# Optimization experiments

Hardware: AMD Instinct MI355X
Metric: run time of the kernel (lower is better)

## Reference

```python
import jax, jax.numpy as jnp
import numpy as np

N = 100000
IN_C = 128
HID = 16
HEADS = 8
OUT_C = 64
E = 1600000
NEG_SLOPE = 0.2
EPS = 1e-16


def setup_inputs() -> dict:
    key = jax.random.key(0)
    ks = jax.random.split(key, 12)
    s = lambda k, shape, fan: jax.random.normal(k, shape, jnp.float32) * (1.0 / np.sqrt(fan))
    return {
        "x": jax.random.normal(ks[0], (N, IN_C), jnp.float32),
        "edge_index": jax.random.randint(ks[1], (2, E), 0, N, jnp.int64),
        # conv1 params (heads=8, concat=True)
        "W1": s(ks[2], (IN_C, HEADS * HID), IN_C),
        "a_src1": s(ks[3], (HEADS, HID), HID),
        "a_dst1": s(ks[4], (HEADS, HID), HID),
        "b1": jnp.zeros((HEADS * HID,), jnp.float32),
        # conv2 params (heads=1, concat=False)
        "W2": s(ks[5], (HEADS * HID, OUT_C), HEADS * HID),
        "a_src2": s(ks[6], (1, OUT_C), OUT_C),
        "a_dst2": s(ks[7], (1, OUT_C), OUT_C),
        "b2": jnp.zeros((OUT_C,), jnp.float32),
    }


def gat_conv(x, src, dst, W, a_src, a_dst, bias, concat):
    """PyG-style GATConv: edge softmax over incoming edges + scatter-add."""
    H, C = a_src.shape
    n = x.shape[0]
    h = (x @ W).reshape(n, H, C)                      # [N,H,C]
    asrc = jnp.einsum("nhc,hc->nh", h, a_src)          # [N,H]
    adst = jnp.einsum("nhc,hc->nh", h, a_dst)          # [N,H]
    e = jax.nn.leaky_relu(asrc[src] + adst[dst], NEG_SLOPE)  # [E,H]
    # numerically-stable segment softmax over edges sharing a destination
    m = jax.ops.segment_max(e, dst, num_segments=n)    # [N,H]
    m = jnp.where(jnp.isfinite(m), m, 0.0)
    ex = jnp.exp(e - m[dst])                           # [E,H]
    denom = jax.ops.segment_sum(ex, dst, num_segments=n)  # [N,H]
    alpha = ex / (denom[dst] + EPS)                    # [E,H]
    out = jax.ops.segment_sum(alpha[:, :, None] * h[src], dst, num_segments=n)  # [N,H,C]
    out = out.reshape(n, H * C) if concat else out.mean(axis=1)
    return out + bias


def reference(x, edge_index, W1, a_src1, a_dst1, b1, W2, a_src2, a_dst2, b2):
    n = x.shape[0]
    # PyG GATConv adds self-loops by default
    loop = jnp.arange(n, dtype=edge_index.dtype)
    src = jnp.concatenate([edge_index[0], loop])
    dst = jnp.concatenate([edge_index[1], loop])
    # dropout(p=0.6) is identity at inference
    h = jax.nn.elu(gat_conv(x, src, dst, W1, a_src1, a_dst1, b1, concat=True))
    return gat_conv(h, src, dst, W2, a_src2, a_dst2, b2, concat=False)
```

## Files before the change

kernel.cpp:

```cpp
#include <hip/hip_runtime.h>
#include <hip/hip_bf16.h>
#include <math.h>


typedef __attribute__((ext_vector_type(8))) short short8;
typedef __attribute__((ext_vector_type(4))) float f32x4;

__device__ __forceinline__ float bflo(uint u) { return __uint_as_float(u << 16); }
__device__ __forceinline__ float bfhi(uint u) { return __uint_as_float(u & 0xffff0000u); }
__device__ __forceinline__ float bf1(ushort v) { return __uint_as_float(((uint)v) << 16); }
__device__ __forceinline__ ushort f2bf(float f) {
    uint u = __float_as_uint(f);
    u += 0x7fff + ((u >> 16) & 1);
    return (ushort)(u >> 16);
}
#define LOG2E 1.44269504088896f
#define CSR_CAP 4096

__global__ __launch_bounds__(256) void k_gemm1_bhist(
    const float* __restrict__ X, const float* __restrict__ W,
    ushort* __restrict__ Y, int n,
    const int* __restrict__ dst, int e, int* __restrict__ bcount, int nbh) {
    __shared__ union {
        struct { ushort As[128][136]; ushort Ws[128][136]; } g;
        int h[1024];
    } sm;
    const int t = threadIdx.x;
    if ((int)blockIdx.x < nbh) {
        for (int i = t; i < 1024; i += 256) sm.h[i] = 0;
        __syncthreads();
        int c0 = blockIdx.x * 8192, c1 = min(c0 + 8192, e);
        for (int i = c0 + t; i < c1; i += 256) atomicAdd(&sm.h[dst[i] >> 7], 1);
        __syncthreads();
        for (int i = t; i < 1024; i += 256)
            if (sm.h[i]) atomicAdd(&bcount[i], sm.h[i]);
        return;
    }
    const int row0 = (blockIdx.x - nbh) * 128;
#pragma unroll
    for (int q = 0; q < 16; q++) {
        int idx = t + q * 256;
        int r = idx >> 5, c4 = (idx & 31) * 4;
        float4 xv = make_float4(0.f, 0.f, 0.f, 0.f);
        if (row0 + r < n) xv = *reinterpret_cast<const float4*>(&X[(size_t)(row0 + r) * 128 + c4]);
        ushort4 w4 = make_ushort4(f2bf(xv.x), f2bf(xv.y), f2bf(xv.z), f2bf(xv.w));
        *reinterpret_cast<ushort4*>(&sm.g.As[r][c4]) = w4;
    }
    for (int i = t; i < 128 * 128; i += 256) {
        int k = i >> 7, nc = i & 127;
        sm.g.Ws[nc][k] = f2bf(W[i]);
    }
    __syncthreads();
    const int w = t >> 6, l = t & 63;
    const int lr = l & 15;
    const int lk = (l >> 4) * 8;
    f32x4 acc[2][8];
#pragma unroll
    for (int m = 0; m < 2; m++)
#pragma unroll
        for (int nb = 0; nb < 8; nb++) acc[m][nb] = (f32x4){0.f, 0.f, 0.f, 0.f};
#pragma unroll
    for (int kc = 0; kc < 128; kc += 32) {
        short8 a0 = *reinterpret_cast<const short8*>(&sm.g.As[w * 32 + lr][kc + lk]);
        short8 a1 = *reinterpret_cast<const short8*>(&sm.g.As[w * 32 + 16 + lr][kc + lk]);
#pragma unroll
        for (int nb = 0; nb < 8; nb++) {
            short8 bf = *reinterpret_cast<const short8*>(&sm.g.Ws[nb * 16 + lr][kc + lk]);
            acc[0][nb] = __builtin_amdgcn_mfma_f32_16x16x32_bf16(a0, bf, acc[0][nb], 0, 0, 0);
            acc[1][nb] = __builtin_amdgcn_mfma_f32_16x16x32_bf16(a1, bf, acc[1][nb], 0, 0, 0);
        }
    }
#pragma unroll
    for (int m = 0; m < 2; m++)
#pragma unroll
        for (int j = 0; j < 4; j++) {
            int r = row0 + w * 32 + m * 16 + (l >> 4) * 4 + j;
            if (r < n) {
#pragma unroll
                for (int nb = 0; nb < 8; nb++)
                    Y[(size_t)r * 128 + nb * 16 + lr] = f2bf(acc[m][nb][j]);
            }
        }
}

__global__ __launch_bounds__(256) void k_bscan_attn1(
    const int* __restrict__ bcount, int nb, int n,
    int* __restrict__ ebase, int* __restrict__ ecur, int* __restrict__ cbase,
    const uint* __restrict__ hu, const float* __restrict__ a_src,
    const float* __restrict__ a_dst, float* __restrict__ asrc,
    float* __restrict__ adst) {
    __shared__ int ae[1024], be[1024], ac[1024], bc[1024];
    int t = threadIdx.x;
    if (blockIdx.x == 0) {
        for (int i = t; i < 1024; i += 256) {
            int v = 0, nn = 0;
            if (i < nb) {
                v = bcount[i];
                nn = min(128, n - (i << 7));
            }
            ae[i] = v;
            ac[i] = v + nn;
        }
        __syncthreads();
        int* pa = ae; int* qa = be; int* pc = ac; int* qc = bc;
        for (int off = 1; off < 1024; off <<= 1) {
            for (int i = t; i < 1024; i += 256) {
                int va = pa[i], vc = pc[i];
                if (i >= off) { va += pa[i - off]; vc += pc[i - off]; }
                qa[i] = va; qc[i] = vc;
            }
            __syncthreads();
            int* tm = pa; pa = qa; qa = tm;
            tm = pc; pc = qc; qc = tm;
        }
        for (int i = t; i < 1024; i += 256) {
            if (i < nb) {
                int ea = (i == 0) ? 0 : pa[i - 1];
                int ca = (i == 0) ? 0 : pc[i - 1];
                ebase[i] = ea; ecur[i] = ea; cbase[i] = ca;
            }
        }
        return;
    }
    int tt = (blockIdx.x - 1) * 256 + t;
    if (tt >= n * 8) return;
    int node = tt >> 3, hd = tt & 7;
    const uint* hp = hu + (size_t)node * 64 + hd * 8;
    float s1 = 0.f, s2 = 0.f;
#pragma unroll
    for (int q = 0; q < 8; q++) {
        uint u = hp[q];
        float v0 = bflo(u), v1 = bfhi(u);
        s1 = fmaf(v0, a_src[hd * 16 + 2 * q], s1);
        s1 = fmaf(v1, a_src[hd * 16 + 2 * q + 1], s1);
        s2 = fmaf(v0, a_dst[hd * 16 + 2 * q], s2);
        s2 = fmaf(v1, a_dst[hd * 16 + 2 * q + 1], s2);
    }
    asrc[tt] = s1 * LOG2E;
    adst[tt] = s2 * LOG2E;
}

__global__ __launch_bounds__(512) void k_part(const int* __restrict__ src,
                                              const int* __restrict__ dst, int e,
                                              int* __restrict__ ecur, int* __restrict__ ebuf) {
    __shared__ int h[1024];
    __shared__ int base[1024];
    int t = threadIdx.x;
    int c0 = blockIdx.x * 8192, c1 = min(c0 + 8192, e);
    for (int i = t; i < 1024; i += 512) h[i] = 0;
    __syncthreads();
    for (int i = c0 + t; i < c1; i += 512) atomicAdd(&h[dst[i] >> 7], 1);
    __syncthreads();
    for (int i = t; i < 1024; i += 512) {
        int c = h[i];
        base[i] = c ? atomicAdd(&ecur[i], c) : 0;
        h[i] = 0;
    }
    __syncthreads();
    for (int i = c0 + t; i < c1; i += 512) {
        int d = dst[i], b = d >> 7;
        int r = atomicAdd(&h[b], 1);
        ebuf[base[b] + r] = (src[i] << 7) | (d & 127);
    }
}

__global__ __launch_bounds__(256) void k_build(const int* __restrict__ ebuf,
                                               const int* __restrict__ bcount,
                                               const int* __restrict__ ebase,
                                               const int* __restrict__ cbase,
                                               int* __restrict__ rowptr,
                                               int* __restrict__ csr, int n, int nb) {
    __shared__ int cnt[128];
    __shared__ int sc[128], sc2[128];
    __shared__ int csr_l[CSR_CAP];
    int b = blockIdx.x, t = threadIdx.x;
    int n0 = b << 7;
    int nn = min(128, n - n0);
    int ec = bcount[b], eb = ebase[b], cb = cbase[b];
    if (t < 128) cnt[t] = 0;
    __syncthreads();
    for (int i = t; i < ec; i += 256) atomicAdd(&cnt[ebuf[eb + i] & 127], 1);
    __syncthreads();
    if (t < 128) sc[t] = (t < nn) ? cnt[t] + 1 : 0;
    __syncthreads();
    int* p = sc; int* q = sc2;
    for (int off = 1; off < 128; off <<= 1) {
        if (t < 128) {
            int v = p[t];
            if (t >= off) v += p[t - off];
            q[t] = v;
        }
        __syncthreads();
        int* tm = p; p = q; q = tm;
    }
    int total = p[127];
    if (total <= CSR_CAP) {
        if (t < nn) {
            int off = (t == 0) ? 0 : p[t - 1];
            rowptr[n0 + t] = cb + off;
            csr_l[off] = n0 + t;
            cnt[t] = off + 1;
        }
        __syncthreads();
        for (int i = t; i < ec; i += 256) {
            int v = ebuf[eb + i];
            int s = atomicAdd(&cnt[v & 127], 1);
            csr_l[s] = v >> 7;
        }
        __syncthreads();
        for (int i = t; i < total; i += 256) csr[cb + i] = csr_l[i];
    } else {
        if (t < nn) {
            int off = (t == 0) ? 0 : p[t - 1];
            rowptr[n0 + t] = cb + off;
            csr[cb + off] = n0 + t;
            cnt[t] = off + 1;
        }
        __syncthreads();
        for (int i = t; i < ec; i += 256) {
            int v = ebuf[eb + i];
            int s = atomicAdd(&cnt[v & 127], 1);
            csr[cb + s] = v >> 7;
        }
    }
    if (b == nb - 1 && t == 0) rowptr[n] = cb + total;
}

__global__ __launch_bounds__(256) void k_gemm2(const ushort* __restrict__ X,
                                               const float* __restrict__ W,
                                               ushort* __restrict__ Y, int n) {
    __shared__ ushort As[128][136];
    __shared__ ushort Ws[64][136];
    const int t = threadIdx.x;
    const int row0 = blockIdx.x * 128;
#pragma unroll
    for (int q = 0; q < 8; q++) {
        int idx = t + q * 256;
        int r = idx >> 4, c8 = (idx & 15) * 8;
        uint4 v = make_uint4(0u, 0u, 0u, 0u);
        if (row0 + r < n) v = *reinterpret_cast<const uint4*>(&X[(size_t)(row0 + r) * 128 + c8]);
        *reinterpret_cast<uint4*>(&As[r][c8]) = v;
    }
    for (int i = t; i < 128 * 64; i += 256) {
        int k = i >> 6, nc = i & 63;
        Ws[nc][k] = f2bf(W[i]);
    }
    __syncthreads();
    const int w = t >> 6, l = t & 63;
    const int lr = l & 15;
    const int lk = (l >> 4) * 8;
    f32x4 acc[2][4];
#pragma unroll
    for (int m = 0; m < 2; m++)
#pragma unroll
        for (int nb = 0; nb < 4; nb++) acc[m][nb] = (f32x4){0.f, 0.f, 0.f, 0.f};
#pragma unroll
    for (int kc = 0; kc < 128; kc += 32) {
        short8 a0 = *reinterpret_cast<const short8*>(&As[w * 32 + lr][kc + lk]);
        short8 a1 = *reinterpret_cast<const short8*>(&As[w * 32 + 16 + lr][kc + lk]);
#pragma unroll
        for (int nb = 0; nb < 4; nb++) {
            short8 bf = *reinterpret_cast<const short8*>(&Ws[nb * 16 + lr][kc + lk]);
            acc[0][nb] = __builtin_amdgcn_mfma_f32_16x16x32_bf16(a0, bf, acc[0][nb], 0, 0, 0);
            acc[1][nb] = __builtin_amdgcn_mfma_f32_16x16x32_bf16(a1, bf, acc[1][nb], 0, 0, 0);
        }
    }
#pragma unroll
    for (int m = 0; m < 2; m++)
#pragma unroll
        for (int j = 0; j < 4; j++) {
            int r = row0 + w * 32 + m * 16 + (l >> 4) * 4 + j;
            if (r < n) {
#pragma unroll
                for (int nb = 0; nb < 4; nb++)
                    Y[(size_t)r * 64 + nb * 16 + lr] = f2bf(acc[m][nb][j]);
            }
        }
}

__global__ void k_attn2(const uint* __restrict__ hu, const float* __restrict__ a_src,
                        const float* __restrict__ a_dst, float* __restrict__ asrc,
                        float* __restrict__ adst, int n) {
    int t = blockIdx.x * 256 + threadIdx.x;
    if (t >= n * 8) return;
    int node = t >> 3, j = t & 7;
    const uint* hp = hu + (size_t)node * 32 + j * 4;
    float s1 = 0.f, s2 = 0.f;
#pragma unroll
    for (int q = 0; q < 4; q++) {
        uint u = hp[q];
        float v0 = bflo(u), v1 = bfhi(u);
        s1 = fmaf(v0, a_src[j * 8 + 2 * q], s1);
        s1 = fmaf(v1, a_src[j * 8 + 2 * q + 1], s1);
        s2 = fmaf(v0, a_dst[j * 8 + 2 * q], s2);
        s2 = fmaf(v1, a_dst[j * 8 + 2 * q + 1], s2);
    }
#pragma unroll
    for (int o = 1; o < 8; o <<= 1) {
        s1 += __shfl_xor(s1, o);
        s2 += __shfl_xor(s2, o);
    }
    if (j == 0) { asrc[node] = s1 * LOG2E; adst[node] = s2 * LOG2E; }
}

__global__ __launch_bounds__(256) void k_agg1(
    const uint* __restrict__ hu, const float* __restrict__ asrc,
    const float* __restrict__ adst, const int* __restrict__ rowptr,
    const int* __restrict__ csr, const float* __restrict__ b1,
    uint* __restrict__ x2, int n) {
    __shared__ float P[4][512];
    int wv = threadIdx.x >> 6;
    int wid = (blockIdx.x * 256 + threadIdx.x) >> 6;
    if (wid >= n) return;
    uint lane = threadIdx.x & 63;
    uint hd = lane >> 3;
    uint sl = lane & 7;
    uint c0 = lane * 2;
    float adn = adst[(uint)wid * 8u + hd];
    int beg = rowptr[wid], end = rowptr[wid + 1];
    float s = 0.f, acc0 = 0.f, acc1 = 0.f;
    for (int base = beg; base < end; base += 64) {
        int cnt = min(64, end - base);
        int vidx = ((int)lane < cnt) ? csr[base + lane] : 0;
        int mb = (cnt + 7) >> 3;
        for (int m = 0; m < mb; m++) {
            int slot = 8 * m + (int)sl;
            int cs = csr[base + min(slot, cnt - 1)];
            float e = asrc[(uint)cs * 8u + hd] + adn;
            e = fmaxf(e, 0.2f * e);
            P[wv][slot * 8 + hd] = exp2f(e);
        }
        asm volatile("s_waitcnt lgkmcnt(0)" ::: "memory");
        int j = 0;
        for (; j + 8 <= cnt; j += 8) {
            uint s0 = __builtin_amdgcn_readlane(vidx, j);
            uint s1 = __builtin_amdgcn_readlane(vidx, j + 1);
            uint s2 = __builtin_amdgcn_readlane(vidx, j + 2);
            uint s3 = __builtin_amdgcn_readlane(vidx, j + 3);
            uint s4 = __builtin_amdgcn_readlane(vidx, j + 4);
            uint s5 = __builtin_amdgcn_readlane(vidx, j + 5);
            uint s6 = __builtin_amdgcn_readlane(vidx, j + 6);
            uint s7 = __builtin_amdgcn_readlane(vidx, j + 7);
            uint u0 = hu[s0 * 64u + lane];
            uint u1 = hu[s1 * 64u + lane];
            uint u2 = hu[s2 * 64u + lane];
            uint u3 = hu[s3 * 64u + lane];
            uint u4 = hu[s4 * 64u + lane];
            uint u5 = hu[s5 * 64u + lane];
            uint u6 = hu[s6 * 64u + lane];
            uint u7 = hu[s7 * 64u + lane];
            float q0 = P[wv][(j + 0) * 8 + hd];
            float q1 = P[wv][(j + 1) * 8 + hd];
            float q2 = P[wv][(j + 2) * 8 + hd];
            float q3 = P[wv][(j + 3) * 8 + hd];
            float q4 = P[wv][(j + 4) * 8 + hd];
            float q5 = P[wv][(j + 5) * 8 + hd];
            float q6 = P[wv][(j + 6) * 8 + hd];
            float q7 = P[wv][(j + 7) * 8 + hd];
            s += ((q0 + q1) + (q2 + q3)) + ((q4 + q5) + (q6 + q7));
            acc0 = fmaf(q0, bflo(u0), fmaf(q1, bflo(u1), acc0));
            acc0 = fmaf(q2, bflo(u2), fmaf(q3, bflo(u3), acc0));
            acc0 = fmaf(q4, bflo(u4), fmaf(q5, bflo(u5), acc0));
            acc0 = fmaf(q6, bflo(u6), fmaf(q7, bflo(u7), acc0));
            acc1 = fmaf(q0, bfhi(u0), fmaf(q1, bfhi(u1), acc1));
            acc1 = fmaf(q2, bfhi(u2), fmaf(q3, bfhi(u3), acc1));
            acc1 = fmaf(q4, bfhi(u4), fmaf(q5, bfhi(u5), acc1));
            acc1 = fmaf(q6, bfhi(u6), fmaf(q7, bfhi(u7), acc1));
        }
        for (; j < cnt; ++j) {
            uint s0 = __builtin_amdgcn_readlane(vidx, j);
            float q0 = P[wv][j * 8 + hd];
            uint u0 = hu[s0 * 64u + lane];
            s += q0;
            acc0 = fmaf(q0, bflo(u0), acc0);
            acc1 = fmaf(q0, bfhi(u0), acc1);
        }
    }
    float inv = 1.f / (s + 1e-16f);
    float o0 = acc0 * inv + b1[c0];
    float o1 = acc1 * inv + b1[c0 + 1];
    o0 = o0 > 0.f ? o0 : (__expf(o0) - 1.f);
    o1 = o1 > 0.f ? o1 : (__expf(o1) - 1.f);
    union { ushort b[2]; uint u; } pk;
    pk.b[0] = f2bf(o0);
    pk.b[1] = f2bf(o1);
    x2[(uint)wid * 64u + lane] = pk.u;
}
__global__ __launch_bounds__(256) void k_agg2(
    const ushort* __restrict__ hb, const float* __restrict__ asrc,
    const float* __restrict__ adst, const int* __restrict__ rowptr,
    const int* __restrict__ csr, const float* __restrict__ b2,
    float* __restrict__ out, int n) {
    __shared__ float P2[4][64];
    int wv = threadIdx.x >> 6;
    int wid = (blockIdx.x * 256 + threadIdx.x) >> 6;
    if (wid >= n) return;
    uint lane = threadIdx.x & 63;
    float adn = adst[wid];
    int beg = rowptr[wid], end = rowptr[wid + 1];
    float s = 0.f, acc = 0.f;
    for (int base = beg; base < end; base += 64) {
        int cnt = min(64, end - base);
        int vidx = csr[base + min((int)lane, cnt - 1)];
        float e = asrc[vidx] + adn;
        e = fmaxf(e, 0.2f * e);
        P2[wv][lane] = ((int)lane < cnt) ? exp2f(e) : 0.f;
        asm volatile("s_waitcnt lgkmcnt(0)" ::: "memory");
        int j = 0;
        for (; j + 8 <= cnt; j += 8) {
            uint s0 = __builtin_amdgcn_readlane(vidx, j);
            uint s1 = __builtin_amdgcn_readlane(vidx, j + 1);
            uint s2 = __builtin_amdgcn_readlane(vidx, j + 2);
            uint s3 = __builtin_amdgcn_readlane(vidx, j + 3);
            uint s4 = __builtin_amdgcn_readlane(vidx, j + 4);
            uint s5 = __builtin_amdgcn_readlane(vidx, j + 5);
            uint s6 = __builtin_amdgcn_readlane(vidx, j + 6);
            uint s7 = __builtin_amdgcn_readlane(vidx, j + 7);
            float h0 = bf1(hb[s0 * 64u + lane]);
            float h1 = bf1(hb[s1 * 64u + lane]);
            float h2 = bf1(hb[s2 * 64u + lane]);
            float h3 = bf1(hb[s3 * 64u + lane]);
            float h4 = bf1(hb[s4 * 64u + lane]);
            float h5 = bf1(hb[s5 * 64u + lane]);
            float h6 = bf1(hb[s6 * 64u + lane]);
            float h7 = bf1(hb[s7 * 64u + lane]);
            float q0 = P2[wv][j + 0];
            float q1 = P2[wv][j + 1];
            float q2 = P2[wv][j + 2];
            float q3 = P2[wv][j + 3];
            float q4 = P2[wv][j + 4];
            float q5 = P2[wv][j + 5];
            float q6 = P2[wv][j + 6];
            float q7 = P2[wv][j + 7];
            s += ((q0 + q1) + (q2 + q3)) + ((q4 + q5) + (q6 + q7));
            acc = fmaf(q0, h0, fmaf(q1, h1, acc));
            acc = fmaf(q2, h2, fmaf(q3, h3, acc));
            acc = fmaf(q4, h4, fmaf(q5, h5, acc));
            acc = fmaf(q6, h6, fmaf(q7, h7, acc));
        }
        for (; j < cnt; ++j) {
            uint s0 = __builtin_amdgcn_readlane(vidx, j);
            float q0 = P2[wv][j];
            float h0 = bf1(hb[s0 * 64u + lane]);
            s += q0;
            acc = fmaf(q0, h0, acc);
        }
    }
    out[(size_t)wid * 64 + lane] = acc / (s + 1e-16f) + b2[lane];
}

extern "C" void kernel_launch(void* const* d_in, const int* in_sizes, int n_in,
                              void* d_out, int out_size, void* d_ws, size_t ws_size,
                              hipStream_t stream) {
    const float* x   = (const float*)d_in[0];
    const int*   ei  = (const int*)d_in[1];
    const float* W1  = (const float*)d_in[2];
    const float* as1 = (const float*)d_in[3];
    const float* ad1 = (const float*)d_in[4];
    const float* b1  = (const float*)d_in[5];
    const float* W2  = (const float*)d_in[6];
    const float* as2 = (const float*)d_in[7];
    const float* ad2 = (const float*)d_in[8];
    const float* b2  = (const float*)d_in[9];
    float* out = (float*)d_out;

    int N = in_sizes[0] / 128;
    int E = in_sizes[1] / 2;
    int TOT = E + N;
    const int* src = ei;
    const int* dst = ei + E;

    char* p = (char*)d_ws;
    auto alloc = [&](size_t bytes) {
        char* r = p;
        p += (bytes + 255) & ~size_t(255);
        return r;
    };
    ushort* h1b  = (ushort*)alloc((size_t)N * 128 * 2);
    ushort* h2b  = (ushort*)alloc((size_t)N * 64 * 2);
    ushort* x2b  = (ushort*)alloc((size_t)N * 128 * 2);
    float* asrc1 = (float*)alloc((size_t)N * 8 * 4);
    float* adst1 = (float*)alloc((size_t)N * 8 * 4);
    float* asrc2 = (float*)alloc((size_t)N * 4);
    float* adst2 = (float*)alloc((size_t)N * 4);
    int* rowptr  = (int*)alloc((size_t)(N + 1) * 4);
    int* csr     = (int*)alloc((size_t)TOT * 4);
    int* ebuf    = (int*)alloc((size_t)E * 4);
    int* bcount  = (int*)alloc(1024 * 4);
    int* ebase   = (int*)alloc(1024 * 4);
    int* ecur    = (int*)alloc(1024 * 4);
    int* cbase   = (int*)alloc(1024 * 4);

    int NB = (N + 127) >> 7;
    int nbp = (E + 8191) / 8192;
    int gb = (N + 127) / 128;

    hipMemsetAsync(bcount, 0, 1024 * 4, stream);
    k_gemm1_bhist<<<nbp + gb, 256, 0, stream>>>(x, W1, h1b, N, dst, E, bcount, nbp);
    k_bscan_attn1<<<1 + (N * 8 + 255) / 256, 256, 0, stream>>>(
        bcount, NB, N, ebase, ecur, cbase, (const uint*)h1b, as1, ad1, asrc1, adst1);
    k_part<<<nbp, 512, 0, stream>>>(src, dst, E, ecur, ebuf);
    k_build<<<NB, 256, 0, stream>>>(ebuf, bcount, ebase, cbase, rowptr, csr, N, NB);
    k_agg1<<<(N + 3) / 4, 256, 0, stream>>>((const uint*)h1b, asrc1, adst1, rowptr, csr, b1,
                                            (uint*)x2b, N);
    k_gemm2<<<gb, 256, 0, stream>>>(x2b, W2, h2b, N);
    k_attn2<<<(N * 8 + 255) / 256, 256, 0, stream>>>((const uint*)h2b, as2, ad2, asrc2, adst2, N);
    k_agg2<<<(N + 3) / 4, 256, 0, stream>>>((const ushort*)h2b, asrc2, adst2, rowptr, csr, b2,
                                            out, N);
}
```

Measured before the change: 235.8 us.

## Precompute layer-1 edge attention weights in CSR build and store as fp16

Moves the per-edge leaky-relu and exp2 computation for layer-1 attention out of the aggregation kernel and into the CSR build kernel. Each edge writes 8 fp16 unnormalised weights in CSR order, and asrc/adst are stored as fp16 to halve their gather traffic. k_agg1 then streams those precomputed weights instead of gathering asrc per edge and staging the results in LDS. The cost is an extra E*16-byte write and read, a second shared array in k_build, and reduced precision from fp16 logits and weights, which could overflow since no max subtraction is applied.

Result: faster. 229.2 us (-2.8%).

```diff
diff --git a/kernel.cpp b/kernel.cpp
--- a/kernel.cpp
+++ b/kernel.cpp
@@ -87,8 +87,8 @@
     const int* __restrict__ bcount, int nb, int n,
     int* __restrict__ ebase, int* __restrict__ ecur, int* __restrict__ cbase,
     const uint* __restrict__ hu, const float* __restrict__ a_src,
-    const float* __restrict__ a_dst, float* __restrict__ asrc,
-    float* __restrict__ adst) {
+    const float* __restrict__ a_dst, _Float16* __restrict__ asrc,
+    _Float16* __restrict__ adst) {
     __shared__ int ae[1024], be[1024], ac[1024], bc[1024];
     int t = threadIdx.x;
     if (blockIdx.x == 0) {
@@ -136,8 +136,8 @@
         s2 = fmaf(v0, a_dst[hd * 16 + 2 * q], s2);
         s2 = fmaf(v1, a_dst[hd * 16 + 2 * q + 1], s2);
     }
-    asrc[tt] = s1 * LOG2E;
-    adst[tt] = s2 * LOG2E;
+    asrc[tt] = (_Float16)(s1 * LOG2E);
+    adst[tt] = (_Float16)(s2 * LOG2E);
 }
 
 __global__ __launch_bounds__(512) void k_part(const int* __restrict__ src,
@@ -168,11 +168,15 @@
                                                const int* __restrict__ bcount,
                                                const int* __restrict__ ebase,
                                                const int* __restrict__ cbase,
+                                               const _Float16* __restrict__ asrc,
+                                               const _Float16* __restrict__ adst,
                                                int* __restrict__ rowptr,
-                                               int* __restrict__ csr, int n, int nb) {
+                                               int* __restrict__ csr,
+                                               _Float16* __restrict__ p1, int n, int nb) {
     __shared__ int cnt[128];
     __shared__ int sc[128], sc2[128];
     __shared__ int csr_l[CSR_CAP];
+    __shared__ int dst_l[CSR_CAP];
     int b = blockIdx.x, t = threadIdx.x;
     int n0 = b << 7;
     int nn = min(128, n - n0);
@@ -199,6 +203,7 @@
             int off = (t == 0) ? 0 : p[t - 1];
             rowptr[n0 + t] = cb + off;
             csr_l[off] = n0 + t;
+            dst_l[off] = n0 + t;
             cnt[t] = off + 1;
         }
         __syncthreads();
@@ -206,21 +211,59 @@
             int v = ebuf[eb + i];
             int s = atomicAdd(&cnt[v & 127], 1);
             csr_l[s] = v >> 7;
-        }
-        __syncthreads();
-        for (int i = t; i < total; i += 256) csr[cb + i] = csr_l[i];
+            dst_l[s] = n0 + (v & 127);
+        }
+        __syncthreads();
+        for (int i = t; i < total; i += 256) {
+            int s = csr_l[i], d = dst_l[i];
+            csr[cb + i] = s;
+            const _Float16* pa = asrc + (size_t)s * 8;
+            const _Float16* pb = adst + (size_t)d * 8;
+            _Float16 buf[8];
+#pragma unroll
+            for (int h = 0; h < 8; h++) {
+                float e = (float)pa[h] + (float)pb[h];
+                e = fmaxf(e, 0.2f * e);
+                buf[h] = (_Float16)exp2f(e);
+            }
+            *reinterpret_cast<uint4*>(&p1[(size_t)(cb + i) * 8]) =
+                *reinterpret_cast<const uint4*>(buf);
+        }
     } else {
         if (t < nn) {
             int off = (t == 0) ? 0 : p[t - 1];
             rowptr[n0 + t] = cb + off;
             csr[cb + off] = n0 + t;
             cnt[t] = off + 1;
+            const _Float16* pa = asrc + (size_t)(n0 + t) * 8;
+            const _Float16* pb = adst + (size_t)(n0 + t) * 8;
+            _Float16 buf[8];
+#pragma unroll
+            for (int h = 0; h < 8; h++) {
+                float e = (float)pa[h] + (float)pb[h];
+                e = fmaxf(e, 0.2f * e);
+                buf[h] = (_Float16)exp2f(e);
+            }
+            *reinterpret_cast<uint4*>(&p1[(size_t)(cb + off) * 8]) =
+                *reinterpret_cast<const uint4*>(buf);
         }
         __syncthreads();
         for (int i = t; i < ec; i += 256) {
             int v = ebuf[eb + i];
+            int sidx = v >> 7, d = n0 + (v & 127);
             int s = atomicAdd(&cnt[v & 127], 1);
-            csr[cb + s] = v >> 7;
+            csr[cb + s] = sidx;
+            const _Float16* pa = asrc + (size_t)sidx * 8;
+            const _Float16* pb = adst + (size_t)d * 8;
+            _Float16 buf[8];
+#pragma unroll
+            for (int h = 0; h < 8; h++) {
+                float e = (float)pa[h] + (float)pb[h];
+                e = fmaxf(e, 0.2f * e);
+                buf[h] = (_Float16)exp2f(e);
+            }
+            *reinterpret_cast<uint4*>(&p1[(size_t)(cb + s) * 8]) =
+                *reinterpret_cast<const uint4*>(buf);
         }
     }
     if (b == nb - 1 && t == 0) rowptr[n] = cb + total;
@@ -304,33 +347,20 @@
 }
 
 __global__ __launch_bounds__(256) void k_agg1(
-    const uint* __restrict__ hu, const float* __restrict__ asrc,
-    const float* __restrict__ adst, const int* __restrict__ rowptr,
-    const int* __restrict__ csr, const float* __restrict__ b1,
-    uint* __restrict__ x2, int n) {
-    __shared__ float P[4][512];
-    int wv = threadIdx.x >> 6;
+    const uint* __restrict__ hu, const _Float16* __restrict__ p1,
+    const int* __restrict__ rowptr, const int* __restrict__ csr,
+    const float* __restrict__ b1, uint* __restrict__ x2, int n) {
     int wid = (blockIdx.x * 256 + threadIdx.x) >> 6;
     if (wid >= n) return;
     uint lane = threadIdx.x & 63;
+    uint c0 = lane * 2;
     uint hd = lane >> 3;
-    uint sl = lane & 7;
-    uint c0 = lane * 2;
-    float adn = adst[(uint)wid * 8u + hd];
     int beg = rowptr[wid], end = rowptr[wid + 1];
     float s = 0.f, acc0 = 0.f, acc1 = 0.f;
     for (int base = beg; base < end; base += 64) {
         int cnt = min(64, end - base);
         int vidx = ((int)lane < cnt) ? csr[base + lane] : 0;
-        int mb = (cnt + 7) >> 3;
-        for (int m = 0; m < mb; m++) {
-            int slot = 8 * m + (int)sl;
-            int cs = csr[base + min(slot, cnt - 1)];
-            float e = asrc[(uint)cs * 8u + hd] + adn;
-            e = fmaxf(e, 0.2f * e);
-            P[wv][slot * 8 + hd] = exp2f(e);
-        }
-        asm volatile("s_waitcnt lgkmcnt(0)" ::: "memory");
+        const _Float16* pp = p1 + (size_t)base * 8 + hd;
         int j = 0;
         for (; j + 8 <= cnt; j += 8) {
             uint s0 = __builtin_amdgcn_readlane(vidx, j);
@@ -349,14 +379,14 @@
             uint u5 = hu[s5 * 64u + lane];
             uint u6 = hu[s6 * 64u + lane];
             uint u7 = hu[s7 * 64u + lane];
-            float q0 = P[wv][(j + 0) * 8 + hd];
-            float q1 = P[wv][(j + 1) * 8 + hd];
-            float q2 = P[wv][(j + 2) * 8 + hd];
-            float q3 = P[wv][(j + 3) * 8 + hd];
-            float q4 = P[wv][(j + 4) * 8 + hd];
-            float q5 = P[wv][(j + 5) * 8 + hd];
-            float q6 = P[wv][(j + 6) * 8 + hd];
-            float q7 = P[wv][(j + 7) * 8 + hd];
+            float q0 = (float)pp[(j + 0) * 8];
+            float q1 = (float)pp[(j + 1) * 8];
+            float q2 = (float)pp[(j + 2) * 8];
+            float q3 = (float)pp[(j + 3) * 8];
+            float q4 = (float)pp[(j + 4) * 8];
+            float q5 = (float)pp[(j + 5) * 8];
+            float q6 = (float)pp[(j + 6) * 8];
+            float q7 = (float)pp[(j + 7) * 8];
             s += ((q0 + q1) + (q2 + q3)) + ((q4 + q5) + (q6 + q7));
             acc0 = fmaf(q0, bflo(u0), fmaf(q1, bflo(u1), acc0));
             acc0 = fmaf(q2, bflo(u2), fmaf(q3, bflo(u3), acc0));
@@ -369,7 +399,7 @@
         }
         for (; j < cnt; ++j) {
             uint s0 = __builtin_amdgcn_readlane(vidx, j);
-            float q0 = P[wv][j * 8 + hd];
+            float q0 = (float)pp[j * 8];
             uint u0 = hu[s0 * 64u + lane];
             s += q0;
             acc0 = fmaf(q0, bflo(u0), acc0);
@@ -386,6 +416,7 @@
     pk.b[1] = f2bf(o1);
     x2[(uint)wid * 64u + lane] = pk.u;
 }
+
 __global__ __launch_bounds__(256) void k_agg2(
     const ushort* __restrict__ hb, const float* __restrict__ asrc,
     const float* __restrict__ adst, const int* __restrict__ rowptr,
@@ -479,13 +510,14 @@
     ushort* h1b  = (ushort*)alloc((size_t)N * 128 * 2);
     ushort* h2b  = (ushort*)alloc((size_t)N * 64 * 2);
     ushort* x2b  = (ushort*)alloc((size_t)N * 128 * 2);
-    float* asrc1 = (float*)alloc((size_t)N * 8 * 4);
-    float* adst1 = (float*)alloc((size_t)N * 8 * 4);
+    _Float16* asrc1 = (_Float16*)alloc((size_t)N * 8 * 2);
+    _Float16* adst1 = (_Float16*)alloc((size_t)N * 8 * 2);
     float* asrc2 = (float*)alloc((size_t)N * 4);
     float* adst2 = (float*)alloc((size_t)N * 4);
     int* rowptr  = (int*)alloc((size_t)(N + 1) * 4);
     int* csr     = (int*)alloc((size_t)TOT * 4);
     int* ebuf    = (int*)alloc((size_t)E * 4);
+    _Float16* p1 = (_Float16*)alloc(((size_t)TOT * 8 + 16) * 2);
     int* bcount  = (int*)alloc(1024 * 4);
     int* ebase   = (int*)alloc(1024 * 4);
     int* ecur    = (int*)alloc(1024 * 4);
@@ -500,8 +532,9 @@
     k_bscan_attn1<<<1 + (N * 8 + 255) / 256, 256, 0, stream>>>(
         bcount, NB, N, ebase, ecur, cbase, (const uint*)h1b, as1, ad1, asrc1, adst1);
     k_part<<<nbp, 512, 0, stream>>>(src, dst, E, ecur, ebuf);
-    k_build<<<NB, 256, 0, stream>>>(ebuf, bcount, ebase, cbase, rowptr, csr, N, NB);
-    k_agg1<<<(N + 3) / 4, 256, 0, stream>>>((const uint*)h1b, asrc1, adst1, rowptr, csr, b1,
+    k_build<<<NB, 256, 0, stream>>>(ebuf, bcount, ebase, cbase, asrc1, adst1,
+                                    rowptr, csr, p1, N, NB);
+    k_agg1<<<(N + 3) / 4, 256, 0, stream>>>((const uint*)h1b, p1, rowptr, csr, b1,
                                             (uint*)x2b, N);
     k_gemm2<<<gb, 256, 0, stream>>>(x2b, W2, h2b, N);
     k_attn2<<<(N * 8 + 255) / 256, 256, 0, stream>>>((const uint*)h2b, as2, ad2, asrc2, adst2, N);
```
